# Kernel tuning notes

Hardware: AMD Instinct MI355X
Metric: run time of the kernel (lower is better)

## Reference

```python
import jax, jax.numpy as jnp
import numpy as np


def deform_conv2d(x, w, offset, mask, pad):
    """Modulated deformable conv (DCNv2), stride 1, dilation 1, groups 1.
    x: [B,C,H,W], w: [Co,C,kh,kw], offset: [B,2*K,H,W] (y,x per tap), mask: [B,K,H,W].
    Output spatial size equals input (pad = (k-1)//2).
    """
    B, C, H, W = x.shape
    Co, _, kh, kw = w.shape
    K = kh * kw
    off = offset.reshape(B, K, 2, H, W)
    dy, dx = off[:, :, 0], off[:, :, 1]               # [B,K,H,W]
    ky, kx = jnp.meshgrid(jnp.arange(kh), jnp.arange(kw), indexing='ij')
    ky = ky.reshape(K).astype(x.dtype)
    kx = kx.reshape(K).astype(x.dtype)
    hh = jnp.arange(H, dtype=x.dtype)
    ww = jnp.arange(W, dtype=x.dtype)
    # sampling coords: p0 + p_k + delta p_k
    py = hh[None, None, :, None] - pad + ky[None, :, None, None] + dy  # [B,K,H,W]
    px = ww[None, None, None, :] - pad + kx[None, :, None, None] + dx
    y0 = jnp.floor(py)
    x0 = jnp.floor(px)
    wy = py - y0
    wx = px - x0
    y0i = y0.astype(jnp.int32)
    x0i = x0.astype(jnp.int32)
    x_flat = x.reshape(B, C, H * W)

    def gather(yi, xi):
        valid = (yi >= 0) & (yi < H) & (xi >= 0) & (xi < W)  # zero padding outside
        idx = jnp.clip(yi, 0, H - 1) * W + jnp.clip(xi, 0, W - 1)
        g = jnp.take_along_axis(x_flat, idx.reshape(B, 1, K * H * W), axis=2)
        g = g.reshape(B, C, K, H, W)
        return g * valid[:, None].astype(x.dtype)

    v00 = gather(y0i, x0i)
    v01 = gather(y0i, x0i + 1)
    v10 = gather(y0i + 1, x0i)
    v11 = gather(y0i + 1, x0i + 1)
    wy_ = wy[:, None]  # [B,1,K,H,W]
    wx_ = wx[:, None]
    samp = (v00 * (1 - wy_) * (1 - wx_) + v01 * (1 - wy_) * wx_
            + v10 * wy_ * (1 - wx_) + v11 * wy_ * wx_)   # [B,C,K,H,W]
    # masked weighted accumulation == conv over sampled taps
    return jnp.einsum('bckhw,bkhw,ock->bohw', samp, mask, w.reshape(Co, C, K))


def setup_inputs() -> dict:
    key = jax.random.key(0)
    ks = jax.random.split(key, 10)
    B, C, H, W, Co = 4, 64, 64, 64, 64
    inp = {
        'x': jax.random.normal(ks[0], (B, C, H, W), dtype=jnp.float32),
        'filter1': jax.random.normal(ks[1], (Co, C, 3, 3), dtype=jnp.float32) * 0.05,
        'offset1': jax.random.normal(ks[2], (B, 2 * 9, H, W), dtype=jnp.float32),
        'mask1': jax.random.uniform(ks[3], (B, 9, H, W), dtype=jnp.float32),
        'filter2': jax.random.normal(ks[4], (Co, C, 5, 5), dtype=jnp.float32) * 0.03,
        'offset2': jax.random.normal(ks[5], (B, 2 * 25, H, W), dtype=jnp.float32),
        'mask2': jax.random.uniform(ks[6], (B, 25, H, W), dtype=jnp.float32),
        'filter3': jax.random.normal(ks[7], (Co, C, 7, 7), dtype=jnp.float32) * 0.02,
        'offset3': jax.random.normal(ks[8], (B, 2 * 49, H, W), dtype=jnp.float32),
        'mask3': jax.random.uniform(ks[9], (B, 49, H, W), dtype=jnp.float32),
    }
    return inp


def reference(x, filter1, offset1, mask1, filter2, offset2, mask2, filter3, offset3, mask3):
    part1 = deform_conv2d(x, filter1, offset1, mask1, pad=1)  # 3x3
    part2 = deform_conv2d(x, filter2, offset2, mask2, pad=2)  # 5x5
    part3 = deform_conv2d(x, filter3, offset3, mask3, pad=3)  # 7x7
    return jnp.concatenate((part1, part2, part3), axis=1)
```

## Files before the change

kernel.cpp:

```cpp
#include <hip/hip_runtime.h>
#include <hip/hip_bf16.h>


typedef __attribute__((ext_vector_type(8))) short bf16x8;
typedef __attribute__((ext_vector_type(8))) unsigned short u16x8;
typedef __attribute__((ext_vector_type(4))) float f32x4;
typedef __attribute__((ext_vector_type(2))) float f32x2;

#define WR 16
#define WC 30
#define WS 68
#define SLS 20

__device__ __forceinline__ unsigned short f2bf(float f) {
    __hip_bfloat16 h = __float2bfloat16(f);
    return *reinterpret_cast<unsigned short*>(&h);
}
__device__ __forceinline__ f32x2 unpk(unsigned u) {
    f32x2 r;
    r[0] = __uint_as_float(u << 16);
    r[1] = __uint_as_float(u & 0xffff0000u);
    return r;
}

__global__ __launch_bounds__(256) void k_prep(
    const float* __restrict__ x,
    const float* __restrict__ f1, const float* __restrict__ f2, const float* __restrict__ f3,
    unsigned short* __restrict__ xTb,
    unsigned short* __restrict__ wp1, unsigned short* __restrict__ wp2, unsigned short* __restrict__ wp3) {
    __shared__ float tile[64][65];
    int bid = blockIdx.x;
    int tid = threadIdx.x;
    if (bid < 256) {
        int b = bid >> 6, h = bid & 63;
        {
            int w = tid & 63, c4 = tid >> 6;
            const float* xp = x + (((b * 64) * 64 + h) * 64) + w;
            #pragma unroll
            for (int i = 0; i < 16; ++i) {
                int c = c4 * 16 + i;
                tile[c][w] = xp[c * 4096];
            }
        }
        __syncthreads();
        {
            int c = tid & 63, w4 = tid >> 6;
            unsigned short* op = xTb + (((b * 64 + h) * 64) * 64) + c;
            #pragma unroll
            for (int i = 0; i < 16; ++i) {
                int ww = w4 * 16 + i;
                op[ww * 64] = f2bf(tile[c][ww]);
            }
        }
    } else {
        int idx = (bid - 256) * 256 + tid;
        const float* f; unsigned short* wp; int K, rel;
        if (idx < 36864)       { f = f1; wp = wp1; K = 9;  rel = idx; }
        else if (idx < 139264) { f = f2; wp = wp2; K = 25; rel = idx - 36864; }
        else                   { f = f3; wp = wp3; K = 49; rel = idx - 139264; }
        int k    = rel >> 12;
        int r2   = rel & 4095;
        int ct   = r2 >> 10;
        int cg   = (r2 >> 9) & 1;
        int lane = (r2 >> 3) & 63;
        int j    = r2 & 7;
        int o = ct * 16 + (lane & 15);
        int c = cg * 32 + (lane >> 4) * 8 + j;
        wp[rel] = f2bf(f[(o * 64 + c) * K + k]);
    }
}

__global__ __launch_bounds__(512, 4) void k_dcn(
    const unsigned short* __restrict__ xTb,
    const float* __restrict__ off1, const float* __restrict__ msk1, const unsigned short* __restrict__ wp1,
    const float* __restrict__ off2, const float* __restrict__ msk2, const unsigned short* __restrict__ wp2,
    const float* __restrict__ off3, const float* __restrict__ msk3, const unsigned short* __restrict__ wp3,
    float* __restrict__ out) {

    __shared__ __align__(16) unsigned char smem[WR * WC * WS * 2];
    unsigned short* win = (unsigned short*)smem;
    float* slab = (float*)smem;

    int tile = blockIdx.x;
    int b  = tile >> 8;
    int h  = (tile >> 2) & 63;
    int w0 = (tile & 3) << 4;

    int tid  = threadIdx.x;
    int wv   = tid >> 6;
    int lane = tid & 63;
    int quad = lane >> 4;
    int l16  = lane & 15;
    int ylo  = h - 7, cxlo = w0 - 7;

    const unsigned short* xb = xTb + ((size_t)b << 18);

    {
        int j = tid & 7;
        for (int p = tid >> 3; p < WR * WC; p += 64) {
            int r = p / WC, cc = p - r * WC;
            int y = min(max(ylo + r, 0), 63);
            int x = min(max(cxlo + cc, 0), 63);
            *(u16x8*)(win + p * WS + j * 8) =
                *(const u16x8*)(xb + (((y << 6) + x) << 6) + j * 8);
        }
    }
    __syncthreads();

    int pw   = w0 + l16;
    int ch0  = quad << 3;
    int lofs = lane << 3;

    const float* offs; const float* msks; const unsigned short* wpF;
    int ks, ke, kw, pad;
    switch (wv) {
        case 0:  offs = off1; msks = msk1; wpF = wp1; kw = 3; pad = 1; ks = 0;  ke = 9;  break;
        case 1:  offs = off2; msks = msk2; wpF = wp2; kw = 5; pad = 2; ks = 0;  ke = 12; break;
        case 2:  offs = off2; msks = msk2; wpF = wp2; kw = 5; pad = 2; ks = 12; ke = 25; break;
        case 3:  offs = off3; msks = msk3; wpF = wp3; kw = 7; pad = 3; ks = 0;  ke = 10; break;
        case 4:  offs = off3; msks = msk3; wpF = wp3; kw = 7; pad = 3; ks = 10; ke = 20; break;
        case 5:  offs = off3; msks = msk3; wpF = wp3; kw = 7; pad = 3; ks = 20; ke = 30; break;
        case 6:  offs = off3; msks = msk3; wpF = wp3; kw = 7; pad = 3; ks = 30; ke = 40; break;
        default: offs = off3; msks = msk3; wpF = wp3; kw = 7; pad = 3; ks = 40; ke = 49; break;
    }
    int K2 = (kw == 3) ? 9 : (kw == 5) ? 25 : 49;
    const float* offp = offs + ((b * 2 * K2) * 4096) + (h << 6) + pw;
    const float* mskp = msks + ((b * K2) * 4096) + (h << 6) + pw;

    f32x4 acc[4];
    #pragma unroll
    for (int i = 0; i < 4; ++i) acc[i] = (f32x4){0.f, 0.f, 0.f, 0.f};

    int ky = ks / kw, kx = ks - ky * kw;

    float dyC = offp[ks * 8192];
    float dxC = offp[ks * 8192 + 4096];
    float mkC = mskp[ks * 4096];

    for (int k = ks; k < ke; ++k) {
        int kn = min(k + 1, ke - 1);
        float dyN = offp[kn * 8192];
        float dxN = offp[kn * 8192 + 4096];
        float mkN = mskp[kn * 4096];

        float py = (float)(h - pad + ky) + dyC;
        float px = (float)(pw - pad + kx) + dxC;
        float y0f = floorf(py), x0f = floorf(px);
        float wy = py - y0f, wx = px - x0f;
        int y0 = (int)y0f, x0 = (int)x0f;
        int y1 = y0 + 1, x1 = x0 + 1;
        float fy0 = ((unsigned)y0 < 64u) ? (1.f - wy) * mkC : 0.f;
        float fy1 = ((unsigned)y1 < 64u) ? wy * mkC         : 0.f;
        float gx0 = ((unsigned)x0 < 64u) ? (1.f - wx)       : 0.f;
        float gx1 = ((unsigned)x1 < 64u) ? wx               : 0.f;
        float w00 = fy0 * gx0, w01 = fy0 * gx1, w10 = fy1 * gx0, w11 = fy1 * gx1;

        int r0 = y0 - ylo, r1 = r0 + 1;
        int c0 = x0 - cxlo, c1 = c0 + 1;
        bool oow = ((w00 != 0.f) & (((unsigned)r0 >= WR) | ((unsigned)c0 >= WC)))
                 | ((w01 != 0.f) & (((unsigned)r0 >= WR) | ((unsigned)c1 >= WC)))
                 | ((w10 != 0.f) & (((unsigned)r1 >= WR) | ((unsigned)c0 >= WC)))
                 | ((w11 != 0.f) & (((unsigned)r1 >= WR) | ((unsigned)c1 >= WC)));
        int r0c = min(max(r0, 0), WR - 1), r1c = min(max(r1, 0), WR - 1);
        int c0c = min(max(c0, 0), WC - 1), c1c = min(max(c1, 0), WC - 1);
        int p00 = (r0c * WC + c0c) * WS;
        int p01 = (r0c * WC + c1c) * WS;
        int p10 = (r1c * WC + c0c) * WS;
        int p11 = (r1c * WC + c1c) * WS;

        union U { u16x8 v; unsigned u[4]; };
        U g00a, g01a, g10a, g11a, g00b, g01b, g10b, g11b;
        g00a.v = *(const u16x8*)(win + p00 + ch0);
        g01a.v = *(const u16x8*)(win + p01 + ch0);
        g10a.v = *(const u16x8*)(win + p10 + ch0);
        g11a.v = *(const u16x8*)(win + p11 + ch0);
        g00b.v = *(const u16x8*)(win + p00 + 32 + ch0);
        g01b.v = *(const u16x8*)(win + p01 + 32 + ch0);
        g10b.v = *(const u16x8*)(win + p10 + 32 + ch0);
        g11b.v = *(const u16x8*)(win + p11 + 32 + ch0);

        if (oow) {
            int y0g = min(max(y0, 0), 63), y1g = min(max(y1, 0), 63);
            int x0g = min(max(x0, 0), 63), x1g = min(max(x1, 0), 63);
            int o00 = ((y0g << 6) + x0g) << 6;
            int o01 = ((y0g << 6) + x1g) << 6;
            int o10 = ((y1g << 6) + x0g) << 6;
            int o11 = ((y1g << 6) + x1g) << 6;
            g00a.v = *(const u16x8*)(xb + o00 + ch0);
            g01a.v = *(const u16x8*)(xb + o01 + ch0);
            g10a.v = *(const u16x8*)(xb + o10 + ch0);
            g11a.v = *(const u16x8*)(xb + o11 + ch0);
            g00b.v = *(const u16x8*)(xb + o00 + 32 + ch0);
            g01b.v = *(const u16x8*)(xb + o01 + 32 + ch0);
            g10b.v = *(const u16x8*)(xb + o10 + 32 + ch0);
            g11b.v = *(const u16x8*)(xb + o11 + 32 + ch0);
        }

        f32x2 W00 = {w00, w00}, W01 = {w01, w01}, W10 = {w10, w10}, W11 = {w11, w11};
        union { bf16x8 v; unsigned short u[8]; } A0, A1;
        #pragma unroll
        for (int j2 = 0; j2 < 4; ++j2) {
            f32x2 s0 = W00 * unpk(g00a.u[j2]) + W01 * unpk(g01a.u[j2])
                     + W10 * unpk(g10a.u[j2]) + W11 * unpk(g11a.u[j2]);
            f32x2 s1 = W00 * unpk(g00b.u[j2]) + W01 * unpk(g01b.u[j2])
                     + W10 * unpk(g10b.u[j2]) + W11 * unpk(g11b.u[j2]);
            A0.u[2 * j2]     = f2bf(s0[0]);
            A0.u[2 * j2 + 1] = f2bf(s0[1]);
            A1.u[2 * j2]     = f2bf(s1[0]);
            A1.u[2 * j2 + 1] = f2bf(s1[1]);
        }

        const unsigned short* wpk = wpF + (k << 12) + lofs;
        #pragma unroll
        for (int ct = 0; ct < 4; ++ct) {
            bf16x8 b0 = *(const bf16x8*)(wpk + ct * 1024);
            bf16x8 b1 = *(const bf16x8*)(wpk + ct * 1024 + 512);
            acc[ct] = __builtin_amdgcn_mfma_f32_16x16x32_bf16(A0.v, b0, acc[ct], 0, 0, 0);
            acc[ct] = __builtin_amdgcn_mfma_f32_16x16x32_bf16(A1.v, b1, acc[ct], 0, 0, 0);
        }

        dyC = dyN; dxC = dxN; mkC = mkN;
        if (++kx == kw) { kx = 0; ++ky; }
    }

    __syncthreads();

    #pragma unroll
    for (int ct = 0; ct < 4; ++ct) {
        *(f32x4*)&slab[wv * 1280 + (ct * 16 + l16) * SLS + quad * 4] = acc[ct];
    }
    __syncthreads();

    for (int it = tid; it < 768; it += 512) {
        int g = it & 3;
        int o = it >> 2;
        int oo = o & 63;
        int base = oo * SLS + g * 4;
        f32x4 v;
        if (o < 64) {
            v = *(const f32x4*)&slab[base];
        } else if (o < 128) {
            f32x4 a0 = *(const f32x4*)&slab[1 * 1280 + base];
            f32x4 a1 = *(const f32x4*)&slab[2 * 1280 + base];
            #pragma unroll
            for (int r = 0; r < 4; ++r) v[r] = a0[r] + a1[r];
        } else {
            f32x4 a0 = *(const f32x4*)&slab[3 * 1280 + base];
            f32x4 a1 = *(const f32x4*)&slab[4 * 1280 + base];
            f32x4 a2 = *(const f32x4*)&slab[5 * 1280 + base];
            f32x4 a3 = *(const f32x4*)&slab[6 * 1280 + base];
            f32x4 a4 = *(const f32x4*)&slab[7 * 1280 + base];
            #pragma unroll
            for (int r = 0; r < 4; ++r) v[r] = (a0[r] + a1[r]) + (a2[r] + a3[r]) + a4[r];
        }
        *(f32x4*)&out[(((size_t)b * 192 + o) * 64 + h) * 64 + w0 + g * 4] = v;
    }
}

extern "C" void kernel_launch(void* const* d_in, const int* in_sizes, int n_in,
                              void* d_out, int out_size, void* d_ws, size_t ws_size,
                              hipStream_t stream) {
    const float* x    = (const float*)d_in[0];
    const float* f1   = (const float*)d_in[1];
    const float* off1 = (const float*)d_in[2];
    const float* msk1 = (const float*)d_in[3];
    const float* f2   = (const float*)d_in[4];
    const float* off2 = (const float*)d_in[5];
    const float* msk2 = (const float*)d_in[6];
    const float* f3   = (const float*)d_in[7];
    const float* off3 = (const float*)d_in[8];
    const float* msk3 = (const float*)d_in[9];
    float* out = (float*)d_out;

    unsigned short* xTb = (unsigned short*)d_ws;
    unsigned short* wp1 = xTb + 4 * 64 * 64 * 64;
    unsigned short* wp2 = wp1 + 9 * 4096;
    unsigned short* wp3 = wp2 + 25 * 4096;

    k_prep<<<dim3(1584), dim3(256), 0, stream>>>(x, f1, f2, f3, xTb, wp1, wp2, wp3);
    k_dcn<<<dim3(1024), dim3(512), 0, stream>>>(xTb,
                                                off1, msk1, wp1,
                                                off2, msk2, wp2,
                                                off3, msk3, wp3,
                                                out);
}
```

Before: 165.4 us.

## Pre-pack offsets and masks per tile, stage them in LDS

The prep kernel gains extra blocks that rearrange the offset and mask arrays into a per-tile contiguous buffer (83 taps × 48 floats per tile). The main kernel copies that buffer into shared memory with vector loads alongside the input window, then reads dy/dx/mask from LDS in the tap loop instead of strided global loads with software prefetch. This trades a second pass over offset/mask data in the prep kernel, plus more LDS per block, for fewer scattered global loads in the tap loop.

```diff
diff --git a/kernel.cpp b/kernel.cpp
--- a/kernel.cpp
+++ b/kernel.cpp
@@ -11,6 +11,7 @@
 #define WC 30
 #define WS 68
 #define SLS 20
+#define PARM_OFF 65280
 
 __device__ __forceinline__ unsigned short f2bf(float f) {
     __hip_bfloat16 h = __float2bfloat16(f);
@@ -26,8 +27,12 @@
 __global__ __launch_bounds__(256) void k_prep(
     const float* __restrict__ x,
     const float* __restrict__ f1, const float* __restrict__ f2, const float* __restrict__ f3,
+    const float* __restrict__ off1, const float* __restrict__ msk1,
+    const float* __restrict__ off2, const float* __restrict__ msk2,
+    const float* __restrict__ off3, const float* __restrict__ msk3,
     unsigned short* __restrict__ xTb,
-    unsigned short* __restrict__ wp1, unsigned short* __restrict__ wp2, unsigned short* __restrict__ wp3) {
+    unsigned short* __restrict__ wp1, unsigned short* __restrict__ wp2, unsigned short* __restrict__ wp3,
+    float* __restrict__ parmT) {
     __shared__ float tile[64][65];
     int bid = blockIdx.x;
     int tid = threadIdx.x;
@@ -52,7 +57,7 @@
                 op[ww * 64] = f2bf(tile[c][ww]);
             }
         }
-    } else {
+    } else if (bid < 1584) {
         int idx = (bid - 256) * 256 + tid;
         const float* f; unsigned short* wp; int K, rel;
         if (idx < 36864)       { f = f1; wp = wp1; K = 9;  rel = idx; }
@@ -67,17 +72,30 @@
         int o = ct * 16 + (lane & 15);
         int c = cg * 32 + (lane >> 4) * 8 + j;
         wp[rel] = f2bf(f[(o * 64 + c) * K + k]);
+    } else {
+        int e = (bid - 1584) * 256 + tid;
+        int t = e / 3984;
+        int r = e - t * 3984;
+        int g = r / 48;
+        int j = r - g * 48;
+        int sel = j >> 4;
+        int l = j & 15;
+        int b = t >> 8, h = (t >> 2) & 63, w0 = (t & 3) << 4;
+        const float* src;
+        if (g < 9)       { int k = g;      src = (sel == 2) ? msk1 + (b * 9  + k) * 4096 : off1 + (((b * 9  + k) << 1) + sel) * 4096; }
+        else if (g < 34) { int k = g - 9;  src = (sel == 2) ? msk2 + (b * 25 + k) * 4096 : off2 + (((b * 25 + k) << 1) + sel) * 4096; }
+        else             { int k = g - 34; src = (sel == 2) ? msk3 + (b * 49 + k) * 4096 : off3 + (((b * 49 + k) << 1) + sel) * 4096; }
+        parmT[e] = src[(h << 6) + w0 + l];
     }
 }
 
 __global__ __launch_bounds__(512, 4) void k_dcn(
     const unsigned short* __restrict__ xTb,
-    const float* __restrict__ off1, const float* __restrict__ msk1, const unsigned short* __restrict__ wp1,
-    const float* __restrict__ off2, const float* __restrict__ msk2, const unsigned short* __restrict__ wp2,
-    const float* __restrict__ off3, const float* __restrict__ msk3, const unsigned short* __restrict__ wp3,
+    const unsigned short* __restrict__ wp1, const unsigned short* __restrict__ wp2,
+    const unsigned short* __restrict__ wp3, const float* __restrict__ parmT,
     float* __restrict__ out) {
 
-    __shared__ __align__(16) unsigned char smem[WR * WC * WS * 2];
+    __shared__ __align__(16) unsigned char smem[PARM_OFF + 83 * 48 * 4];
     unsigned short* win = (unsigned short*)smem;
     float* slab = (float*)smem;
 
@@ -105,27 +123,30 @@
                 *(const u16x8*)(xb + (((y << 6) + x) << 6) + j * 8);
         }
     }
+    {
+        const f32x4* psrc = (const f32x4*)(parmT + (size_t)tile * 3984);
+        f32x4* pdst = (f32x4*)(smem + PARM_OFF);
+        for (int i = tid; i < 996; i += 512) pdst[i] = psrc[i];
+    }
     __syncthreads();
 
     int pw   = w0 + l16;
     int ch0  = quad << 3;
     int lofs = lane << 3;
 
-    const float* offs; const float* msks; const unsigned short* wpF;
-    int ks, ke, kw, pad;
+    const unsigned short* wpF;
+    int ks, ke, kw, pad, gbase;
     switch (wv) {
-        case 0:  offs = off1; msks = msk1; wpF = wp1; kw = 3; pad = 1; ks = 0;  ke = 9;  break;
-        case 1:  offs = off2; msks = msk2; wpF = wp2; kw = 5; pad = 2; ks = 0;  ke = 12; break;
-        case 2:  offs = off2; msks = msk2; wpF = wp2; kw = 5; pad = 2; ks = 12; ke = 25; break;
-        case 3:  offs = off3; msks = msk3; wpF = wp3; kw = 7; pad = 3; ks = 0;  ke = 10; break;
-        case 4:  offs = off3; msks = msk3; wpF = wp3; kw = 7; pad = 3; ks = 10; ke = 20; break;
-        case 5:  offs = off3; msks = msk3; wpF = wp3; kw = 7; pad = 3; ks = 20; ke = 30; break;
-        case 6:  offs = off3; msks = msk3; wpF = wp3; kw = 7; pad = 3; ks = 30; ke = 40; break;
-        default: offs = off3; msks = msk3; wpF = wp3; kw = 7; pad = 3; ks = 40; ke = 49; break;
-    }
-    int K2 = (kw == 3) ? 9 : (kw == 5) ? 25 : 49;
-    const float* offp = offs + ((b * 2 * K2) * 4096) + (h << 6) + pw;
-    const float* mskp = msks + ((b * K2) * 4096) + (h << 6) + pw;
+        case 0:  wpF = wp1; kw = 3; pad = 1; ks = 0;  ke = 9;  gbase = 0;  break;
+        case 1:  wpF = wp2; kw = 5; pad = 2; ks = 0;  ke = 12; gbase = 9;  break;
+        case 2:  wpF = wp2; kw = 5; pad = 2; ks = 12; ke = 25; gbase = 21; break;
+        case 3:  wpF = wp3; kw = 7; pad = 3; ks = 0;  ke = 10; gbase = 34; break;
+        case 4:  wpF = wp3; kw = 7; pad = 3; ks = 10; ke = 20; gbase = 44; break;
+        case 5:  wpF = wp3; kw = 7; pad = 3; ks = 20; ke = 30; gbase = 54; break;
+        case 6:  wpF = wp3; kw = 7; pad = 3; ks = 30; ke = 40; gbase = 64; break;
+        default: wpF = wp3; kw = 7; pad = 3; ks = 40; ke = 49; gbase = 74; break;
+    }
+    const float* plw = (const float*)(smem + PARM_OFF) + (gbase - ks) * 48;
 
     f32x4 acc[4];
     #pragma unroll
@@ -133,26 +154,22 @@
 
     int ky = ks / kw, kx = ks - ky * kw;
 
-    float dyC = offp[ks * 8192];
-    float dxC = offp[ks * 8192 + 4096];
-    float mkC = mskp[ks * 4096];
-
     for (int k = ks; k < ke; ++k) {
-        int kn = min(k + 1, ke - 1);
-        float dyN = offp[kn * 8192];
-        float dxN = offp[kn * 8192 + 4096];
-        float mkN = mskp[kn * 4096];
-
-        float py = (float)(h - pad + ky) + dyC;
-        float px = (float)(pw - pad + kx) + dxC;
+        const float* pl = plw + k * 48;
+        float dy = pl[l16];
+        float dx = pl[16 + l16];
+        float mk = pl[32 + l16];
+
+        float py = (float)(h - pad + ky) + dy;
+        float px = (float)(pw - pad + kx) + dx;
         float y0f = floorf(py), x0f = floorf(px);
         float wy = py - y0f, wx = px - x0f;
         int y0 = (int)y0f, x0 = (int)x0f;
         int y1 = y0 + 1, x1 = x0 + 1;
-        float fy0 = ((unsigned)y0 < 64u) ? (1.f - wy) * mkC : 0.f;
-        float fy1 = ((unsigned)y1 < 64u) ? wy * mkC         : 0.f;
-        float gx0 = ((unsigned)x0 < 64u) ? (1.f - wx)       : 0.f;
-        float gx1 = ((unsigned)x1 < 64u) ? wx               : 0.f;
+        float fy0 = ((unsigned)y0 < 64u) ? (1.f - wy) * mk : 0.f;
+        float fy1 = ((unsigned)y1 < 64u) ? wy * mk         : 0.f;
+        float gx0 = ((unsigned)x0 < 64u) ? (1.f - wx)      : 0.f;
+        float gx1 = ((unsigned)x1 < 64u) ? wx              : 0.f;
         float w00 = fy0 * gx0, w01 = fy0 * gx1, w10 = fy1 * gx0, w11 = fy1 * gx1;
 
         int r0 = y0 - ylo, r1 = r0 + 1;
@@ -219,7 +236,6 @@
             acc[ct] = __builtin_amdgcn_mfma_f32_16x16x32_bf16(A1.v, b1, acc[ct], 0, 0, 0);
         }
 
-        dyC = dyN; dxC = dxN; mkC = mkN;
         if (++kx == kw) { kx = 0; ++ky; }
     }
 
@@ -276,11 +292,10 @@
     unsigned short* wp1 = xTb + 4 * 64 * 64 * 64;
     unsigned short* wp2 = wp1 + 9 * 4096;
     unsigned short* wp3 = wp2 + 25 * 4096;
-
-    k_prep<<<dim3(1584), dim3(256), 0, stream>>>(x, f1, f2, f3, xTb, wp1, wp2, wp3);
-    k_dcn<<<dim3(1024), dim3(512), 0, stream>>>(xTb,
-                                                off1, msk1, wp1,
-                                                off2, msk2, wp2,
-                                                off3, msk3, wp3,
-                                                out);
-}
+    float* parmT = (float*)(wp3 + 49 * 4096);
+
+    k_prep<<<dim3(17520), dim3(256), 0, stream>>>(x, f1, f2, f3,
+                                                  off1, msk1, off2, msk2, off3, msk3,
+                                                  xTb, wp1, wp2, wp3, parmT);
+    k_dcn<<<dim3(1024), dim3(512), 0, stream>>>(xTb, wp1, wp2, wp3, parmT, out);
+}
```

After: 175.9 us. 1.06x slower.
